# Optimization experiments

Measured on AMD Instinct MI355X. Metric: run time of the kernel, lower is better.

The kernel has to match this reference:

```python
import jax, jax.numpy as jnp
import numpy as np

N_NODES = 100000
N_EDGES = 3200000
N_FEAT = 128
EMBED = 20
N_CLASSES = 10
N_GRAPHS = 64


def setup_inputs() -> dict:
    key = jax.random.key(0)
    ks = jax.random.split(key, 8)
    x = jax.random.normal(ks[0], (N_NODES, N_FEAT), dtype=jnp.float32)
    edge_index = jax.random.randint(ks[1], (2, N_EDGES), 0, N_NODES, dtype=jnp.int64)
    edge_weights = jax.random.uniform(ks[2], (N_EDGES,), dtype=jnp.float32)
    batch = jnp.sort(jax.random.randint(ks[3], (N_NODES,), 0, N_GRAPHS, dtype=jnp.int64))
    # GCNConv parameters (glorot-ish scale) and final linear layer
    W = jax.random.normal(ks[4], (N_FEAT, EMBED), dtype=jnp.float32) * (1.0 / np.sqrt(N_FEAT))
    b = jnp.zeros((EMBED,), dtype=jnp.float32)
    lin_W = jax.random.normal(ks[5], (2 * EMBED, N_CLASSES), dtype=jnp.float32) * (1.0 / np.sqrt(2 * EMBED))
    lin_b = jnp.zeros((N_CLASSES,), dtype=jnp.float32)
    return {"x": x, "edge_index": edge_index, "edge_weights": edge_weights,
            "batch": batch, "W": W, "b": b, "lin_W": lin_W, "lin_b": lin_b}


def reference(x, edge_index, edge_weights, batch, W, b, lin_W, lin_b):
    N = x.shape[0]
    # --- GCNConv with self-loops and symmetric normalization (PyG semantics) ---
    loops = jnp.arange(N, dtype=edge_index.dtype)
    src = jnp.concatenate([edge_index[0], loops])
    dst = jnp.concatenate([edge_index[1], loops])
    w = jnp.concatenate([edge_weights, jnp.ones((N,), dtype=edge_weights.dtype)])
    deg = jax.ops.segment_sum(w, dst, num_segments=N)  # degree at targets
    dinv = jnp.where(deg > 0, jax.lax.rsqrt(deg), 0.0)
    norm = dinv[src] * w * dinv[dst]  # [E+N]
    xw = x @ W  # [N, EMBED]
    msg = xw[src] * norm[:, None]  # gather + scale
    out1 = jax.ops.segment_sum(msg, dst, num_segments=N) + b  # scatter-add
    # --- L2 normalize per node (F.normalize p=2 dim=1, eps=1e-12), then ReLU ---
    nrm = jnp.sqrt(jnp.sum(out1 * out1, axis=1, keepdims=True))
    embed = jax.nn.relu(out1 / jnp.maximum(nrm, 1e-12))
    # --- global max / mean pool per graph ---
    mx = jax.ops.segment_max(embed, batch, num_segments=N_GRAPHS)
    mx = jnp.where(jnp.isfinite(mx), mx, 0.0)  # empty graphs -> 0
    cnt = jax.ops.segment_sum(jnp.ones((N,), dtype=embed.dtype), batch, num_segments=N_GRAPHS)
    mean = jax.ops.segment_sum(embed, batch, num_segments=N_GRAPHS) / jnp.maximum(cnt, 1.0)[:, None]
    pooled = jnp.concatenate([mx, mean], axis=-1)  # [G, 2*EMBED]
    return pooled @ lin_W + lin_b
```

## Files before the change

kernel.cpp:

```cpp
#include <hip/hip_runtime.h>
#include <hip/hip_fp16.h>

#define NN 100000
#define NE 3200000
#define NF 128
#define EM 20
#define NC 10
#define NG 64

#define NB 782
#define CAPB 4608
#define T 4096
#define SBLK 1024

__global__ __launch_bounds__(SBLK) void k_scatter(
        const int* __restrict__ src, const int* __restrict__ dst,
        const float* __restrict__ w, int* __restrict__ gcursor,
        uint2* __restrict__ barr) {
    __shared__ unsigned int cnt[1024];
    __shared__ unsigned int off[1024];
    __shared__ unsigned int gbase[NB];
    __shared__ unsigned int wsum[16];
    __shared__ uint2 staged[T];
    __shared__ unsigned short bkt[T];
    int tid = threadIdx.x;
    long E0 = (long)blockIdx.x * T;
    int tot = (int)min((long)T, (long)NE - E0);
    cnt[tid] = 0;
    __syncthreads();
    unsigned int dreg[T / SBLK];
#pragma unroll
    for (int k = 0; k < T / SBLK; ++k) {
        int e = k * SBLK + tid;
        dreg[k] = 0;
        if (e < tot) {
            dreg[k] = (unsigned)dst[E0 + e];
            atomicAdd(&cnt[dreg[k] >> 7], 1u);
        }
    }
    __syncthreads();
    {
        int lane = tid & 63, wv = tid >> 6;
        unsigned int v = cnt[tid];
        unsigned int s = v;
#pragma unroll
        for (int o = 1; o < 64; o <<= 1) {
            unsigned int t = __shfl_up(s, o);
            if (lane >= o) s += t;
        }
        if (lane == 63) wsum[wv] = s;
        __syncthreads();
        if (tid == 0) {
            unsigned int a = 0;
#pragma unroll
            for (int i = 0; i < 16; ++i) { unsigned int t = wsum[i]; wsum[i] = a; a += t; }
        }
        __syncthreads();
        off[tid] = wsum[wv] + s - v;
    }
    __syncthreads();
    if (tid < NB) {
        unsigned int c = cnt[tid];
        gbase[tid] = c ? (unsigned int)atomicAdd(&gcursor[tid], (int)c) : 0u;
        cnt[tid] = 0;
    }
    __syncthreads();
#pragma unroll
    for (int k = 0; k < T / SBLK; ++k) {
        int e = k * SBLK + tid;
        if (e < tot) {
            long ge = E0 + e;
            unsigned int d = dreg[k];
            unsigned int b = d >> 7;
            unsigned int slot = atomicAdd(&cnt[b], 1u);
            unsigned int pos = off[b] + slot;
            staged[pos] = make_uint2((((unsigned)src[ge]) << 7) | (d & 127u),
                                     __float_as_uint(w[ge]));
            bkt[pos] = (unsigned short)b;
        }
    }
    __syncthreads();
    for (int i = tid; i < tot; i += SBLK) {
        unsigned int b = bkt[i];
        unsigned int gpos = gbase[b] + ((unsigned)i - off[b]);
        if (gpos < CAPB) barr[(size_t)b * CAPB + gpos] = staged[i];
    }
}

__global__ void k_degb(const int* __restrict__ gcursor, const uint2* __restrict__ barr,
                       float* __restrict__ dinv) {
    __shared__ float dacc[128];
    int bk = blockIdx.x, tid = threadIdx.x;
    if (tid < 128) dacc[tid] = 0.f;
    __syncthreads();
    int cntb = min(gcursor[bk], CAPB);
    const uint2* row = barr + (size_t)bk * CAPB;
    for (int i = tid; i < cntb; i += 1024) {
        uint2 r = row[i];
        atomicAdd(&dacc[r.x & 127u], __uint_as_float(r.y));
    }
    __syncthreads();
    if (tid < 128) {
        int gd = bk * 128 + tid;
        if (gd < NN) dinv[gd] = rsqrtf(1.0f + dacc[tid]);
    }
}

__global__ void k_xw(const float* __restrict__ x, const float* __restrict__ W,
                     const float* __restrict__ dinv,
                     __half* __restrict__ xwhA, __half* __restrict__ xwhB) {
    __shared__ float xs[64 * 129];
    __shared__ float Ws[NF * EM];
    int base = blockIdx.x * 64;
    for (int i = threadIdx.x; i < NF * EM; i += 256) Ws[i] = W[i];
    const float4* xg = (const float4*)(x + (size_t)base * NF);
    for (int v = threadIdx.x; v < 64 * NF / 4; v += 256) {
        int fidx = v * 4;
        size_t gidx = (size_t)base * NF + fidx;
        float4 val = (gidx + 3 < (size_t)NN * NF) ? xg[v] : make_float4(0.f, 0.f, 0.f, 0.f);
        int r = fidx / NF, c = fidx % NF;
        float* p = xs + r * 129 + c;
        p[0] = val.x; p[1] = val.y; p[2] = val.z; p[3] = val.w;
    }
    __syncthreads();
    int n = threadIdx.x & 63;
    int jg = threadIdx.x >> 6;
    int j0 = jg * 5;
    if (base + n >= NN) return;
    float acc[5] = {0.f, 0.f, 0.f, 0.f, 0.f};
    const float* xr = xs + n * 129;
#pragma unroll 4
    for (int k = 0; k < NF; ++k) {
        float xv = xr[k];
        const float* wr = Ws + k * EM + j0;
#pragma unroll
        for (int jj = 0; jj < 5; ++jj) acc[jj] = fmaf(xv, wr[jj], acc[jj]);
    }
    float dv = dinv[base + n];
#pragma unroll
    for (int jj = 0; jj < 5; ++jj) {
        int j = j0 + jj;
        __half hv = __float2half(acc[jj] * dv);
        if (j < 16) xwhA[(size_t)(base + n) * 16 + j] = hv;
        else        xwhB[(size_t)(base + n) * 4 + (j - 16)] = hv;
    }
}

__device__ inline void unpack16(uint4 a0, uint4 a1, float* f) {
    const __half2* h = (const __half2*)&a0;
#pragma unroll
    for (int c = 0; c < 4; ++c) { float2 t = __half22float2(h[c]); f[2*c] = t.x; f[2*c+1] = t.y; }
    h = (const __half2*)&a1;
#pragma unroll
    for (int c = 0; c < 4; ++c) { float2 t = __half22float2(h[c]); f[8+2*c] = t.x; f[9+2*c] = t.y; }
}
__device__ inline void unpack4(uint2 b0, float* f) {
    const __half2* h = (const __half2*)&b0;
#pragma unroll
    for (int c = 0; c < 2; ++c) { float2 t = __half22float2(h[c]); f[2*c] = t.x; f[2*c+1] = t.y; }
}

__global__ void k_sortaggr(const int* __restrict__ gcursor,
                           const unsigned long long* __restrict__ barr64,
                           const __half* __restrict__ xwhA, const __half* __restrict__ xwhB,
                           const float* __restrict__ dinv, const float* __restrict__ b,
                           float* __restrict__ embed) {
    __shared__ unsigned long long srt[CAPB];
    __shared__ unsigned int cnt[128];
    __shared__ unsigned int off[128];
    __shared__ unsigned int wtot;
    int bk = blockIdx.x, tid = threadIdx.x;
    if (tid < 128) cnt[tid] = 0;
    __syncthreads();
    int cntb = min(gcursor[bk], CAPB);
    const unsigned long long* row = barr64 + (size_t)bk * CAPB;
    unsigned long long rec[9];
    unsigned int pos[9];
    int K = 0;
    for (int e = tid; e < cntb; e += 512) {
        rec[K] = row[e];
        pos[K] = atomicAdd(&cnt[(unsigned)rec[K] & 127u], 1u);
        ++K;
    }
    __syncthreads();
    unsigned int v = 0, s = 0;
    if (tid < 128) {
        v = cnt[tid]; s = v;
#pragma unroll
        for (int o = 1; o < 64; o <<= 1) {
            unsigned int t = __shfl_up(s, o);
            if ((tid & 63) >= o) s += t;
        }
        if (tid == 63) wtot = s;
    }
    __syncthreads();
    if (tid < 128) {
        if (tid >= 64) s += wtot;
        off[tid] = s;
    }
    __syncthreads();
    for (int k = 0; k < K; ++k) {
        unsigned int dl = (unsigned)rec[k] & 127u;
        srt[off[dl] - cnt[dl] + pos[k]] = rec[k];
    }
    __syncthreads();
    int d = tid >> 2, sub = tid & 3;
    int s0 = (int)(off[d] - cnt[d]), s1 = (int)off[d];
    const uint4* pA = (const uint4*)xwhA;
    const uint2* pB = (const uint2*)xwhB;
    float acc[20];
#pragma unroll
    for (int j = 0; j < 20; ++j) acc[j] = 0.f;
    for (int e = s0 + sub; e < s1; e += 4) {
        unsigned long long r = srt[e];
        unsigned int sN = ((unsigned int)r) >> 7;
        float nw = __uint_as_float((unsigned int)(r >> 32));
        uint4 a0 = pA[(size_t)sN * 2];
        uint4 a1 = pA[(size_t)sN * 2 + 1];
        uint2 b0 = pB[sN];
        float f[20];
        unpack16(a0, a1, f);
        unpack4(b0, f + 16);
#pragma unroll
        for (int j = 0; j < 20; ++j) acc[j] = fmaf(f[j], nw, acc[j]);
    }
#pragma unroll
    for (int j = 0; j < 20; ++j) {
        acc[j] += __shfl_xor(acc[j], 1);
        acc[j] += __shfl_xor(acc[j], 2);
    }
    if (sub == 0) {
        int gd = bk * 128 + d;
        if (gd < NN) {
            float dv = dinv[gd];
            uint4 a0 = pA[(size_t)gd * 2];
            uint4 a1 = pA[(size_t)gd * 2 + 1];
            uint2 b0 = pB[gd];
            float xdh[20];
            unpack16(a0, a1, xdh);
            unpack4(b0, xdh + 16);
            float r[20];
            float ss = 0.f;
#pragma unroll
            for (int j = 0; j < 20; ++j) {
                r[j] = dv * (acc[j] + xdh[j]) + b[j];
                ss = fmaf(r[j], r[j], ss);
            }
            float inv = 1.0f / fmaxf(sqrtf(ss), 1e-12f);
            float4 o4[5];
            float* o = (float*)o4;
#pragma unroll
            for (int j = 0; j < 20; ++j) {
                float e2 = r[j] * inv;
                o[j] = e2 > 0.f ? e2 : 0.f;
            }
            float4* eo = (float4*)(embed + (size_t)gd * EM);
#pragma unroll
            for (int c = 0; c < 5; ++c) eo[c] = o4[c];
        }
    }
}

__device__ inline int lbound(const int* __restrict__ batch, int key) {
    int lo = 0, hi = NN;
    while (lo < hi) {
        int mid = (lo + hi) >> 1;
        if (batch[mid] < key) lo = mid + 1; else hi = mid;
    }
    return lo;
}

__global__ void k_poolfinal(const float* __restrict__ embed, const int* __restrict__ batch,
                            const float* __restrict__ lw, const float* __restrict__ lb,
                            float* __restrict__ out) {
    __shared__ float cross[4][40];
    __shared__ float pooled[40];
    int g = blockIdx.x;
    int s0 = lbound(batch, g), s1 = lbound(batch, g + 1);
    int cnt = s1 - s0;
    float mx[EM], sm[EM];
#pragma unroll
    for (int j = 0; j < EM; ++j) { mx[j] = 0.f; sm[j] = 0.f; }
    for (int n = s0 + threadIdx.x; n < s1; n += 256) {
        const float4* e = (const float4*)(embed + (size_t)n * EM);
#pragma unroll
        for (int c = 0; c < 5; ++c) {
            float4 v = e[c];
            int j = c * 4;
            mx[j+0] = fmaxf(mx[j+0], v.x); sm[j+0] += v.x;
            mx[j+1] = fmaxf(mx[j+1], v.y); sm[j+1] += v.y;
            mx[j+2] = fmaxf(mx[j+2], v.z); sm[j+2] += v.z;
            mx[j+3] = fmaxf(mx[j+3], v.w); sm[j+3] += v.w;
        }
    }
#pragma unroll
    for (int o = 32; o > 0; o >>= 1) {
#pragma unroll
        for (int j = 0; j < EM; ++j) {
            mx[j] = fmaxf(mx[j], __shfl_xor(mx[j], o));
            sm[j] += __shfl_xor(sm[j], o);
        }
    }
    int wave = threadIdx.x >> 6, lane = threadIdx.x & 63;
    if (lane == 0) {
#pragma unroll
        for (int j = 0; j < EM; ++j) { cross[wave][j] = mx[j]; cross[wave][EM + j] = sm[j]; }
    }
    __syncthreads();
    if (threadIdx.x < 40) {
        int j = threadIdx.x;
        float v = cross[0][j];
        if (j < EM) v = fmaxf(fmaxf(v, cross[1][j]), fmaxf(cross[2][j], cross[3][j]));
        else        v = v + cross[1][j] + cross[2][j] + cross[3][j];
        if (j >= EM) v *= 1.0f / fmaxf((float)cnt, 1.0f);
        pooled[j] = v;
    }
    __syncthreads();
    if (threadIdx.x < NC) {
        int c = threadIdx.x;
        float acc = lb[c];
#pragma unroll
        for (int j = 0; j < 2 * EM; ++j) acc = fmaf(pooled[j], lw[j * NC + c], acc);
        out[g * NC + c] = acc;
    }
}

static inline size_t align_up(size_t v) { return (v + 1023) & ~(size_t)1023; }

extern "C" void kernel_launch(void* const* d_in, const int* in_sizes, int n_in,
                              void* d_out, int out_size, void* d_ws, size_t ws_size,
                              hipStream_t stream) {
    const float* x     = (const float*)d_in[0];
    const int*   ei    = (const int*)d_in[1];
    const float* ew    = (const float*)d_in[2];
    const int*   batch = (const int*)d_in[3];
    const float* W     = (const float*)d_in[4];
    const float* b     = (const float*)d_in[5];
    const float* lw    = (const float*)d_in[6];
    const float* lb    = (const float*)d_in[7];
    float* out = (float*)d_out;

    char* ws = (char*)d_ws;
    int*    gcursor = (int*)ws;    ws += align_up(4096);
    float*  dinv    = (float*)ws;  ws += align_up((size_t)NN * 4);
    __half* xwhA    = (__half*)ws; ws += align_up((size_t)NN * 16 * 2);
    __half* xwhB    = (__half*)ws; ws += align_up((size_t)NN * 4 * 2);
    float*  embed   = (float*)ws;  ws += align_up((size_t)NN * EM * 4);
    uint2*  barr    = (uint2*)ws;
    unsigned long long* barr64 = (unsigned long long*)barr;

    const int* srcp = ei;
    const int* dstp = ei + NE;

    (void)hipMemsetAsync(gcursor, 0, 4096, stream);
    k_scatter<<<(NE + T - 1) / T, SBLK, 0, stream>>>(srcp, dstp, ew, gcursor, barr);
    k_degb<<<NB, 1024, 0, stream>>>(gcursor, barr, dinv);
    k_xw<<<(NN + 63) / 64, 256, 0, stream>>>(x, W, dinv, xwhA, xwhB);
    k_sortaggr<<<NB, 512, 0, stream>>>(gcursor, barr64, xwhA, xwhB, dinv, b, embed);
    k_poolfinal<<<NG, 256, 0, stream>>>(embed, batch, lw, lb, out);
}
```

Baseline: 264.9 us.

## Fuse degree computation into scatter via global atomics and widen aggregation blocks

Removes the separate degree kernel by having the scatter kernel atomically add edge weights into a global degree array, which is zeroed in the same memset as the cursors. The rsqrt is now computed where the degree is consumed, in the xw and aggregation kernels. The aggregation kernel moves to 1024 threads with 8 lanes per destination node, and the unpack-then-FMA step is fused into a single loop. The trade is 3.2M global float atomics into a scattered 100K-entry array in exchange for one fewer pass over the bucketed edge array.

```diff
diff --git a/kernel.cpp b/kernel.cpp
--- a/kernel.cpp
+++ b/kernel.cpp
@@ -16,7 +16,7 @@
 __global__ __launch_bounds__(SBLK) void k_scatter(
         const int* __restrict__ src, const int* __restrict__ dst,
         const float* __restrict__ w, int* __restrict__ gcursor,
-        uint2* __restrict__ barr) {
+        uint2* __restrict__ barr, float* __restrict__ deg) {
     __shared__ unsigned int cnt[1024];
     __shared__ unsigned int off[1024];
     __shared__ unsigned int gbase[NB];
@@ -29,13 +29,17 @@
     cnt[tid] = 0;
     __syncthreads();
     unsigned int dreg[T / SBLK];
+    float wreg[T / SBLK];
 #pragma unroll
     for (int k = 0; k < T / SBLK; ++k) {
         int e = k * SBLK + tid;
         dreg[k] = 0;
+        wreg[k] = 0.f;
         if (e < tot) {
             dreg[k] = (unsigned)dst[E0 + e];
+            wreg[k] = w[E0 + e];
             atomicAdd(&cnt[dreg[k] >> 7], 1u);
+            atomicAdd(&deg[dreg[k]], wreg[k]);
         }
     }
     __syncthreads();
@@ -75,7 +79,7 @@
             unsigned int slot = atomicAdd(&cnt[b], 1u);
             unsigned int pos = off[b] + slot;
             staged[pos] = make_uint2((((unsigned)src[ge]) << 7) | (d & 127u),
-                                     __float_as_uint(w[ge]));
+                                     __float_as_uint(wreg[k]));
             bkt[pos] = (unsigned short)b;
         }
     }
@@ -87,27 +91,8 @@
     }
 }
 
-__global__ void k_degb(const int* __restrict__ gcursor, const uint2* __restrict__ barr,
-                       float* __restrict__ dinv) {
-    __shared__ float dacc[128];
-    int bk = blockIdx.x, tid = threadIdx.x;
-    if (tid < 128) dacc[tid] = 0.f;
-    __syncthreads();
-    int cntb = min(gcursor[bk], CAPB);
-    const uint2* row = barr + (size_t)bk * CAPB;
-    for (int i = tid; i < cntb; i += 1024) {
-        uint2 r = row[i];
-        atomicAdd(&dacc[r.x & 127u], __uint_as_float(r.y));
-    }
-    __syncthreads();
-    if (tid < 128) {
-        int gd = bk * 128 + tid;
-        if (gd < NN) dinv[gd] = rsqrtf(1.0f + dacc[tid]);
-    }
-}
-
 __global__ void k_xw(const float* __restrict__ x, const float* __restrict__ W,
-                     const float* __restrict__ dinv,
+                     const float* __restrict__ deg,
                      __half* __restrict__ xwhA, __half* __restrict__ xwhB) {
     __shared__ float xs[64 * 129];
     __shared__ float Ws[NF * EM];
@@ -136,7 +121,7 @@
 #pragma unroll
         for (int jj = 0; jj < 5; ++jj) acc[jj] = fmaf(xv, wr[jj], acc[jj]);
     }
-    float dv = dinv[base + n];
+    float dv = rsqrtf(1.0f + deg[base + n]);
 #pragma unroll
     for (int jj = 0; jj < 5; ++jj) {
         int j = j0 + jj;
@@ -160,10 +145,11 @@
     for (int c = 0; c < 2; ++c) { float2 t = __half22float2(h[c]); f[2*c] = t.x; f[2*c+1] = t.y; }
 }
 
-__global__ void k_sortaggr(const int* __restrict__ gcursor,
+__global__ __launch_bounds__(1024, 8) void k_sortaggr(
+                           const int* __restrict__ gcursor,
                            const unsigned long long* __restrict__ barr64,
                            const __half* __restrict__ xwhA, const __half* __restrict__ xwhB,
-                           const float* __restrict__ dinv, const float* __restrict__ b,
+                           const float* __restrict__ deg, const float* __restrict__ b,
                            float* __restrict__ embed) {
     __shared__ unsigned long long srt[CAPB];
     __shared__ unsigned int cnt[128];
@@ -174,10 +160,10 @@
     __syncthreads();
     int cntb = min(gcursor[bk], CAPB);
     const unsigned long long* row = barr64 + (size_t)bk * CAPB;
-    unsigned long long rec[9];
-    unsigned int pos[9];
+    unsigned long long rec[5];
+    unsigned int pos[5];
     int K = 0;
-    for (int e = tid; e < cntb; e += 512) {
+    for (int e = tid; e < cntb; e += 1024) {
         rec[K] = row[e];
         pos[K] = atomicAdd(&cnt[(unsigned)rec[K] & 127u], 1u);
         ++K;
@@ -204,54 +190,71 @@
         srt[off[dl] - cnt[dl] + pos[k]] = rec[k];
     }
     __syncthreads();
-    int d = tid >> 2, sub = tid & 3;
+    int d = tid >> 3, sub = tid & 7;
     int s0 = (int)(off[d] - cnt[d]), s1 = (int)off[d];
     const uint4* pA = (const uint4*)xwhA;
     const uint2* pB = (const uint2*)xwhB;
     float acc[20];
 #pragma unroll
     for (int j = 0; j < 20; ++j) acc[j] = 0.f;
-    for (int e = s0 + sub; e < s1; e += 4) {
+    for (int e = s0 + sub; e < s1; e += 8) {
         unsigned long long r = srt[e];
         unsigned int sN = ((unsigned int)r) >> 7;
         float nw = __uint_as_float((unsigned int)(r >> 32));
         uint4 a0 = pA[(size_t)sN * 2];
         uint4 a1 = pA[(size_t)sN * 2 + 1];
         uint2 b0 = pB[sN];
-        float f[20];
-        unpack16(a0, a1, f);
-        unpack4(b0, f + 16);
-#pragma unroll
-        for (int j = 0; j < 20; ++j) acc[j] = fmaf(f[j], nw, acc[j]);
+        const __half2* h0 = (const __half2*)&a0;
+#pragma unroll
+        for (int c = 0; c < 4; ++c) {
+            float2 t = __half22float2(h0[c]);
+            acc[2*c]   = fmaf(t.x, nw, acc[2*c]);
+            acc[2*c+1] = fmaf(t.y, nw, acc[2*c+1]);
+        }
+        const __half2* h1 = (const __half2*)&a1;
+#pragma unroll
+        for (int c = 0; c < 4; ++c) {
+            float2 t = __half22float2(h1[c]);
+            acc[8+2*c]   = fmaf(t.x, nw, acc[8+2*c]);
+            acc[9+2*c]   = fmaf(t.y, nw, acc[9+2*c]);
+        }
+        const __half2* h2 = (const __half2*)&b0;
+#pragma unroll
+        for (int c = 0; c < 2; ++c) {
+            float2 t = __half22float2(h2[c]);
+            acc[16+2*c] = fmaf(t.x, nw, acc[16+2*c]);
+            acc[17+2*c] = fmaf(t.y, nw, acc[17+2*c]);
+        }
     }
 #pragma unroll
     for (int j = 0; j < 20; ++j) {
         acc[j] += __shfl_xor(acc[j], 1);
         acc[j] += __shfl_xor(acc[j], 2);
+        acc[j] += __shfl_xor(acc[j], 4);
     }
     if (sub == 0) {
         int gd = bk * 128 + d;
         if (gd < NN) {
-            float dv = dinv[gd];
+            float dv = rsqrtf(1.0f + deg[gd]);
             uint4 a0 = pA[(size_t)gd * 2];
             uint4 a1 = pA[(size_t)gd * 2 + 1];
             uint2 b0 = pB[gd];
             float xdh[20];
             unpack16(a0, a1, xdh);
             unpack4(b0, xdh + 16);
-            float r[20];
             float ss = 0.f;
 #pragma unroll
             for (int j = 0; j < 20; ++j) {
-                r[j] = dv * (acc[j] + xdh[j]) + b[j];
-                ss = fmaf(r[j], r[j], ss);
+                float r = fmaf(dv, acc[j] + xdh[j], b[j]);
+                acc[j] = r;
+                ss = fmaf(r, r, ss);
             }
             float inv = 1.0f / fmaxf(sqrtf(ss), 1e-12f);
             float4 o4[5];
             float* o = (float*)o4;
 #pragma unroll
             for (int j = 0; j < 20; ++j) {
-                float e2 = r[j] * inv;
+                float e2 = acc[j] * inv;
                 o[j] = e2 > 0.f ? e2 : 0.f;
             }
             float4* eo = (float4*)(embed + (size_t)gd * EM);
@@ -342,7 +345,7 @@
 
     char* ws = (char*)d_ws;
     int*    gcursor = (int*)ws;    ws += align_up(4096);
-    float*  dinv    = (float*)ws;  ws += align_up((size_t)NN * 4);
+    float*  deg     = (float*)ws;  ws += align_up((size_t)NN * 4);
     __half* xwhA    = (__half*)ws; ws += align_up((size_t)NN * 16 * 2);
     __half* xwhB    = (__half*)ws; ws += align_up((size_t)NN * 4 * 2);
     float*  embed   = (float*)ws;  ws += align_up((size_t)NN * EM * 4);
@@ -352,10 +355,9 @@
     const int* srcp = ei;
     const int* dstp = ei + NE;
 
-    (void)hipMemsetAsync(gcursor, 0, 4096, stream);
-    k_scatter<<<(NE + T - 1) / T, SBLK, 0, stream>>>(srcp, dstp, ew, gcursor, barr);
-    k_degb<<<NB, 1024, 0, stream>>>(gcursor, barr, dinv);
-    k_xw<<<(NN + 63) / 64, 256, 0, stream>>>(x, W, dinv, xwhA, xwhB);
-    k_sortaggr<<<NB, 512, 0, stream>>>(gcursor, barr64, xwhA, xwhB, dinv, b, embed);
+    (void)hipMemsetAsync(gcursor, 0, align_up(4096) + align_up((size_t)NN * 4), stream);
+    k_scatter<<<(NE + T - 1) / T, SBLK, 0, stream>>>(srcp, dstp, ew, gcursor, barr, deg);
+    k_xw<<<(NN + 63) / 64, 256, 0, stream>>>(x, W, deg, xwhA, xwhB);
+    k_sortaggr<<<NB, 1024, 0, stream>>>(gcursor, barr64, xwhA, xwhB, deg, b, embed);
     k_poolfinal<<<NG, 256, 0, stream>>>(embed, batch, lw, lb, out);
 }
```

Result: slower. 395.9 us (+49.5%).

## Move XW ahead of degree pass, fold memset into it, apply dinv[src] in aggregation

Applied to the files above, without the earlier changes.

The x@W kernel no longer depends on dinv. It runs first, zeroes the bucket cursors itself (replacing the separate memset), and reads W directly from global memory with a wave-uniform column offset instead of staging it in shared memory. The source-side normalisation dinv[src] moves into the aggregation loop as an extra gathered load per edge, and the self-loop term is scaled explicitly. This removes one launch and the memset node but adds a random 4-byte gather per edge in the hot aggregation loop.

```diff
diff --git a/kernel.cpp b/kernel.cpp
--- a/kernel.cpp
+++ b/kernel.cpp
@@ -12,6 +12,49 @@
 #define CAPB 4608
 #define T 4096
 #define SBLK 1024
+
+__global__ __launch_bounds__(256) void k_xw(
+        const float* __restrict__ x, const float* __restrict__ W,
+        __half* __restrict__ xwhA, __half* __restrict__ xwhB,
+        int* __restrict__ gcursor) {
+    __shared__ float xs[64 * 129];
+    int tid = threadIdx.x;
+    if (blockIdx.x == 0) {
+        for (int i = tid; i < 1024; i += 256) gcursor[i] = 0;
+    }
+    int base = blockIdx.x * 64;
+    const float4* xg = (const float4*)(x + (size_t)base * NF);
+    for (int v = tid; v < 64 * NF / 4; v += 256) {
+        int fidx = v * 4;
+        size_t gidx = (size_t)base * NF + fidx;
+        float4 val = (gidx + 3 < (size_t)NN * NF) ? xg[v] : make_float4(0.f, 0.f, 0.f, 0.f);
+        int r = fidx >> 7, c = fidx & 127;
+        float* p = xs + r * 129 + c;
+        p[0] = val.x; p[1] = val.y; p[2] = val.z; p[3] = val.w;
+    }
+    __syncthreads();
+    int n = tid & 63;
+    int jg = tid >> 6;
+    int j0 = __builtin_amdgcn_readfirstlane(jg) * 5;
+    int node = base + n;
+    if (node >= NN) return;
+    float acc[5] = {0.f, 0.f, 0.f, 0.f, 0.f};
+    const float* xr = xs + n * 129;
+#pragma unroll 4
+    for (int k = 0; k < NF; ++k) {
+        float xv = xr[k];
+        const float* wr = W + k * EM + j0;
+#pragma unroll
+        for (int jj = 0; jj < 5; ++jj) acc[jj] = fmaf(xv, wr[jj], acc[jj]);
+    }
+#pragma unroll
+    for (int jj = 0; jj < 5; ++jj) {
+        int j = j0 + jj;
+        __half hv = __float2half(acc[jj]);
+        if (j < 16) xwhA[(size_t)node * 16 + j] = hv;
+        else        xwhB[(size_t)node * 4 + (j - 16)] = hv;
+    }
+}
 
 __global__ __launch_bounds__(SBLK) void k_scatter(
         const int* __restrict__ src, const int* __restrict__ dst,
@@ -106,46 +149,6 @@
     }
 }
 
-__global__ void k_xw(const float* __restrict__ x, const float* __restrict__ W,
-                     const float* __restrict__ dinv,
-                     __half* __restrict__ xwhA, __half* __restrict__ xwhB) {
-    __shared__ float xs[64 * 129];
-    __shared__ float Ws[NF * EM];
-    int base = blockIdx.x * 64;
-    for (int i = threadIdx.x; i < NF * EM; i += 256) Ws[i] = W[i];
-    const float4* xg = (const float4*)(x + (size_t)base * NF);
-    for (int v = threadIdx.x; v < 64 * NF / 4; v += 256) {
-        int fidx = v * 4;
-        size_t gidx = (size_t)base * NF + fidx;
-        float4 val = (gidx + 3 < (size_t)NN * NF) ? xg[v] : make_float4(0.f, 0.f, 0.f, 0.f);
-        int r = fidx / NF, c = fidx % NF;
-        float* p = xs + r * 129 + c;
-        p[0] = val.x; p[1] = val.y; p[2] = val.z; p[3] = val.w;
-    }
-    __syncthreads();
-    int n = threadIdx.x & 63;
-    int jg = threadIdx.x >> 6;
-    int j0 = jg * 5;
-    if (base + n >= NN) return;
-    float acc[5] = {0.f, 0.f, 0.f, 0.f, 0.f};
-    const float* xr = xs + n * 129;
-#pragma unroll 4
-    for (int k = 0; k < NF; ++k) {
-        float xv = xr[k];
-        const float* wr = Ws + k * EM + j0;
-#pragma unroll
-        for (int jj = 0; jj < 5; ++jj) acc[jj] = fmaf(xv, wr[jj], acc[jj]);
-    }
-    float dv = dinv[base + n];
-#pragma unroll
-    for (int jj = 0; jj < 5; ++jj) {
-        int j = j0 + jj;
-        __half hv = __float2half(acc[jj] * dv);
-        if (j < 16) xwhA[(size_t)(base + n) * 16 + j] = hv;
-        else        xwhB[(size_t)(base + n) * 4 + (j - 16)] = hv;
-    }
-}
-
 __device__ inline void unpack16(uint4 a0, uint4 a1, float* f) {
     const __half2* h = (const __half2*)&a0;
 #pragma unroll
@@ -214,7 +217,7 @@
     for (int e = s0 + sub; e < s1; e += 4) {
         unsigned long long r = srt[e];
         unsigned int sN = ((unsigned int)r) >> 7;
-        float nw = __uint_as_float((unsigned int)(r >> 32));
+        float nw = __uint_as_float((unsigned int)(r >> 32)) * dinv[sN];
         uint4 a0 = pA[(size_t)sN * 2];
         uint4 a1 = pA[(size_t)sN * 2 + 1];
         uint2 b0 = pB[sN];
@@ -243,7 +246,7 @@
             float ss = 0.f;
 #pragma unroll
             for (int j = 0; j < 20; ++j) {
-                r[j] = dv * (acc[j] + xdh[j]) + b[j];
+                r[j] = dv * (acc[j] + xdh[j] * dv) + b[j];
                 ss = fmaf(r[j], r[j], ss);
             }
             float inv = 1.0f / fmaxf(sqrtf(ss), 1e-12f);
@@ -352,10 +355,9 @@
     const int* srcp = ei;
     const int* dstp = ei + NE;
 
-    (void)hipMemsetAsync(gcursor, 0, 4096, stream);
+    k_xw<<<(NN + 63) / 64, 256, 0, stream>>>(x, W, xwhA, xwhB, gcursor);
     k_scatter<<<(NE + T - 1) / T, SBLK, 0, stream>>>(srcp, dstp, ew, gcursor, barr);
     k_degb<<<NB, 1024, 0, stream>>>(gcursor, barr, dinv);
-    k_xw<<<(NN + 63) / 64, 256, 0, stream>>>(x, W, dinv, xwhA, xwhB);
     k_sortaggr<<<NB, 512, 0, stream>>>(gcursor, barr64, xwhA, xwhB, dinv, b, embed);
     k_poolfinal<<<NG, 256, 0, stream>>>(embed, batch, lw, lb, out);
 }
```

After: 276.9 us. 4.5% more time.
